# Optimization experiments

Hardware: AMD Instinct MI355X
Metric: run time of the kernel (lower is better)

The kernel has to match this reference:

```python
import jax, jax.numpy as jnp
import numpy as np

B, S, D, H, F = 4, 1024, 1024, 16, 4096
DH = D // H  # 64


def _xavier(key, shape):
    fan_in, fan_out = shape[-2], shape[-1]
    limit = np.sqrt(6.0 / (fan_in + fan_out)).astype(np.float32)
    return jax.random.uniform(key, shape, jnp.float32, -limit, limit)


def setup_inputs() -> dict:
    key = jax.random.key(0)
    ks = jax.random.split(key, 24)
    inp = {
        'decoder_input': jax.random.normal(ks[0], (B, S, D), jnp.float32),
        'encoder_output': jax.random.normal(ks[1], (B, S, D), jnp.float32),
        'mask': jnp.broadcast_to(jnp.tril(jnp.ones((S, S), jnp.bool_)), (B, S, S)),
    }
    # self-attention per-head Q/K/V weights stacked over heads: (H, D, DH)
    for i, p in enumerate(['sa', 'ca']):
        base = 2 + i * 8
        inp[f'{p}_wq'] = _xavier(ks[base + 0], (H, D, DH))
        inp[f'{p}_wk'] = _xavier(ks[base + 1], (H, D, DH))
        inp[f'{p}_wv'] = _xavier(ks[base + 2], (H, D, DH))
        inp[f'{p}_bq'] = jnp.zeros((H, DH), jnp.float32)
        inp[f'{p}_bk'] = jnp.zeros((H, DH), jnp.float32)
        inp[f'{p}_bv'] = jnp.zeros((H, DH), jnp.float32)
        inp[f'{p}_wo'] = _xavier(ks[base + 3], (H * DH, D))
        inp[f'{p}_bo'] = jnp.zeros((D,), jnp.float32)
    inp['ff_w1'] = _xavier(ks[18], (D, F))
    inp['ff_b1'] = jnp.zeros((F,), jnp.float32)
    inp['ff_w2'] = _xavier(ks[19], (F, D))
    inp['ff_b2'] = jnp.zeros((D,), jnp.float32)
    for j in (1, 2, 3):
        inp[f'ln{j}_g'] = jnp.ones((D,), jnp.float32)
        inp[f'ln{j}_b'] = jnp.zeros((D,), jnp.float32)
    return inp


def _layernorm(x, g, b, eps=1e-12):
    # torch x.var() default is unbiased (ddof=1) -- match it
    mean = jnp.mean(x, axis=-1, keepdims=True)
    var = jnp.var(x, axis=-1, keepdims=True, ddof=1)
    return g * (x - mean) * jax.lax.rsqrt(var + eps) + b


def _mha(q_in, k_in, v_in, wq, bq, wk, bk, wv, bv, wo, bo, mask=None):
    scale = np.float32(1.0 / np.sqrt(DH))
    q = jnp.einsum('bsd,hde->bhse', q_in, wq) + bq[None, :, None, :]
    k = jnp.einsum('bsd,hde->bhse', k_in, wk) + bk[None, :, None, :]
    v = jnp.einsum('bsd,hde->bhse', v_in, wv) + bv[None, :, None, :]
    scores = jnp.einsum('bhqe,bhke->bhqk', q, k) * scale
    if mask is not None:
        scores = jnp.where(mask[:, None, :, :], scores, jnp.float32(-1e9))
    attn = jax.nn.softmax(scores, axis=-1)
    out = jnp.einsum('bhqk,bhke->bhqe', attn, v)  # (B,H,S,DH)
    out = out.transpose(0, 2, 1, 3).reshape(q_in.shape[0], q_in.shape[1], H * DH)
    return out @ wo + bo


def reference(decoder_input, encoder_output, mask,
              sa_wq, sa_wk, sa_wv, sa_bq, sa_bk, sa_bv, sa_wo, sa_bo,
              ca_wq, ca_wk, ca_wv, ca_bq, ca_bk, ca_bv, ca_wo, ca_bo,
              ff_w1, ff_b1, ff_w2, ff_b2,
              ln1_g, ln1_b, ln2_g, ln2_b, ln3_g, ln3_b):
    # dropout is identity (eval mode)
    out1 = _mha(decoder_input, decoder_input, decoder_input,
                sa_wq, sa_bq, sa_wk, sa_bk, sa_wv, sa_bv, sa_wo, sa_bo, mask)
    out1 = _layernorm(out1 + decoder_input, ln1_g, ln1_b)
    out2 = _mha(out1, encoder_output, encoder_output,
                ca_wq, ca_bq, ca_wk, ca_bk, ca_wv, ca_bv, ca_wo, ca_bo, None)
    out2 = _layernorm(out2 + out1, ln2_g, ln2_b)
    out3 = jax.nn.relu(out2 @ ff_w1 + ff_b1) @ ff_w2 + ff_b2
    out3 = _layernorm(out3 + out2, ln3_g, ln3_b)
    return out3
```

## Files before the change

kernel.cpp:

```cpp
#include <hip/hip_runtime.h>
#include <hip/hip_bf16.h>

using bf16 = __hip_bfloat16;
typedef __attribute__((ext_vector_type(8))) short bf16x8;
typedef __attribute__((ext_vector_type(4))) float f32x4;

__device__ __forceinline__ float toF(float x) { return x; }
__device__ __forceinline__ float toF(bf16 x) { return __bfloat162float(x); }

template <typename T> __device__ __forceinline__ T fromF(float x);
template <> __device__ __forceinline__ float fromF<float>(float x) { return x; }
template <> __device__ __forceinline__ bf16 fromF<bf16>(float x) { return __float2bfloat16(x); }

__device__ __forceinline__ unsigned short f2bu(float f) {
    bf16 h = __float2bfloat16(f);
    return *reinterpret_cast<unsigned short*>(&h);
}

__global__ __launch_bounds__(256) void cvt_k(const float* __restrict__ X,
                                             unsigned short* __restrict__ Y, int n)
{
    int i = (blockIdx.x * 256 + threadIdx.x) * 4;
    if (i >= n) return;
    float4 v = *(const float4*)(X + i);
    ushort4 o;
    o.x = f2bu(v.x); o.y = f2bu(v.y); o.z = f2bu(v.z); o.w = f2bu(v.w);
    *(ushort4*)(Y + i) = o;
}

template <bool HEADED>
__global__ __launch_bounds__(256) void wtrans_k(
    const float* __restrict__ W, unsigned short* __restrict__ Wt, int K, int N)
{
    __shared__ float t[32][33];
    const int k0 = blockIdx.x * 32, n0 = blockIdx.y * 32;
    const int tx = threadIdx.x & 31, ty = threadIdx.x >> 5;
#pragma unroll
    for (int i = 0; i < 4; i++) {
        int k = k0 + ty + 8 * i, n = n0 + tx;
        float v;
        if constexpr (HEADED) v = W[((size_t)(n >> 6) * K + k) * 64 + (n & 63)];
        else                  v = W[(size_t)k * N + n];
        t[ty + 8 * i][tx] = v;
    }
    __syncthreads();
#pragma unroll
    for (int i = 0; i < 4; i++)
        Wt[(size_t)(n0 + ty + 8 * i) * K + k0 + tx] = f2bu(t[tx][ty + 8 * i]);
}

template <typename TO, typename TR, bool RELU, bool HASRES, bool TRANSC, bool NARROW>
__global__ __launch_bounds__(256) void gemm_mfma(
    const unsigned short* __restrict__ A, const unsigned short* __restrict__ Bt,
    const float* __restrict__ bias, const TR* __restrict__ res,
    TO* __restrict__ C, int M, int N, int K)
{
    constexpr int P = 56;
    constexpr int BN = NARROW ? 64 : 128;
    constexpr int MI = NARROW ? 2 : 4;
    __shared__ __align__(16) unsigned short As[128 * P];
    __shared__ __align__(16) unsigned short Bs[BN * P];

    const int tid = threadIdx.x;
    const int lane = tid & 63, wv = tid >> 6;
    const int quad = lane >> 4, col = lane & 15;
    const int m0 = blockIdx.y * 128, n0 = blockIdx.x * BN;
    const int wm = NARROW ? wv * 32 : (wv >> 1) * 64;
    const int wn = NARROW ? 0 : (wv & 1) * 64;

    f32x4 acc[MI][4];
#pragma unroll
    for (int i = 0; i < MI; i++)
#pragma unroll
        for (int j = 0; j < 4; j++) acc[i][j] = (f32x4){0.f, 0.f, 0.f, 0.f};

    const int r0 = tid >> 2;
    const int sg = (tid & 3) * 8;

    for (int k0 = 0; k0 < K; k0 += 32) {
        bf16x8 a0 = *(const bf16x8*)(A  + (size_t)(m0 + r0)      * K + k0 + sg);
        bf16x8 a1 = *(const bf16x8*)(A  + (size_t)(m0 + 64 + r0) * K + k0 + sg);
        bf16x8 b0 = *(const bf16x8*)(Bt + (size_t)(n0 + r0)      * K + k0 + sg);
        bf16x8 b1{};
        if constexpr (!NARROW)
            b1 = *(const bf16x8*)(Bt + (size_t)(n0 + 64 + r0) * K + k0 + sg);
        __syncthreads();
        *(bf16x8*)(As + r0 * P + sg)        = a0;
        *(bf16x8*)(As + (64 + r0) * P + sg) = a1;
        *(bf16x8*)(Bs + r0 * P + sg)        = b0;
        if constexpr (!NARROW)
            *(bf16x8*)(Bs + (64 + r0) * P + sg) = b1;
        __syncthreads();

        bf16x8 af[MI], bf[4];
#pragma unroll
        for (int mi = 0; mi < MI; mi++)
            af[mi] = *(const bf16x8*)(As + (wm + mi * 16 + col) * P + quad * 8);
#pragma unroll
        for (int ni = 0; ni < 4; ni++)
            bf[ni] = *(const bf16x8*)(Bs + (wn + ni * 16 + col) * P + quad * 8);
#pragma unroll
        for (int mi = 0; mi < MI; mi++)
#pragma unroll
            for (int ni = 0; ni < 4; ni++)
                acc[mi][ni] = __builtin_amdgcn_mfma_f32_16x16x32_bf16(
                    af[mi], bf[ni], acc[mi][ni], 0, 0, 0);
    }

    float bv[4];
#pragma unroll
    for (int ni = 0; ni < 4; ni++) bv[ni] = bias[n0 + wn + ni * 16 + col];
#pragma unroll
    for (int mi = 0; mi < MI; mi++) {
#pragma unroll
        for (int r = 0; r < 4; r++) {
            int m = m0 + wm + mi * 16 + quad * 4 + r;
#pragma unroll
            for (int ni = 0; ni < 4; ni++) {
                int n = n0 + wn + ni * 16 + col;
                float v = acc[mi][ni][r] + bv[ni];
                if constexpr (HASRES) v += toF(res[(size_t)m * N + n]);
                if constexpr (RELU) v = v > 0.f ? v : 0.f;
                if constexpr (TRANSC)
                    C[((size_t)(m >> 10) * 1024 + n) * 1024 + (m & 1023)] = fromF<TO>(v);
                else
                    C[(size_t)m * N + n] = fromF<TO>(v);
            }
        }
    }
}

struct SegArgs {
    const float* bias[3];
    unsigned short* out[3];
};

__global__ __launch_bounds__(256) void gemm_seg(
    const unsigned short* __restrict__ A, const unsigned short* __restrict__ Bt,
    SegArgs sp, int M, int K, int transSeg)
{
    constexpr int P = 56;
    __shared__ __align__(16) unsigned short As[128 * P];
    __shared__ __align__(16) unsigned short Bs[128 * P];

    const int tid = threadIdx.x;
    const int lane = tid & 63, wv = tid >> 6;
    const int quad = lane >> 4, col = lane & 15;
    const int m0 = blockIdx.y * 128, n0 = blockIdx.x * 128;
    const int wm = (wv >> 1) * 64, wn = (wv & 1) * 64;

    f32x4 acc[4][4];
#pragma unroll
    for (int i = 0; i < 4; i++)
#pragma unroll
        for (int j = 0; j < 4; j++) acc[i][j] = (f32x4){0.f, 0.f, 0.f, 0.f};

    const int r0 = tid >> 2;
    const int sg = (tid & 3) * 8;

    for (int k0 = 0; k0 < K; k0 += 32) {
        bf16x8 a0 = *(const bf16x8*)(A  + (size_t)(m0 + r0)      * K + k0 + sg);
        bf16x8 a1 = *(const bf16x8*)(A  + (size_t)(m0 + 64 + r0) * K + k0 + sg);
        bf16x8 b0 = *(const bf16x8*)(Bt + (size_t)(n0 + r0)      * K + k0 + sg);
        bf16x8 b1 = *(const bf16x8*)(Bt + (size_t)(n0 + 64 + r0) * K + k0 + sg);
        __syncthreads();
        *(bf16x8*)(As + r0 * P + sg)        = a0;
        *(bf16x8*)(As + (64 + r0) * P + sg) = a1;
        *(bf16x8*)(Bs + r0 * P + sg)        = b0;
        *(bf16x8*)(Bs + (64 + r0) * P + sg) = b1;
        __syncthreads();

        bf16x8 af[4], bf[4];
#pragma unroll
        for (int mi = 0; mi < 4; mi++)
            af[mi] = *(const bf16x8*)(As + (wm + mi * 16 + col) * P + quad * 8);
#pragma unroll
        for (int ni = 0; ni < 4; ni++)
            bf[ni] = *(const bf16x8*)(Bs + (wn + ni * 16 + col) * P + quad * 8);
#pragma unroll
        for (int mi = 0; mi < 4; mi++)
#pragma unroll
            for (int ni = 0; ni < 4; ni++)
                acc[mi][ni] = __builtin_amdgcn_mfma_f32_16x16x32_bf16(
                    af[mi], bf[ni], acc[mi][ni], 0, 0, 0);
    }

    const int seg = n0 >> 10;
    const float* bias = sp.bias[seg];
    unsigned short* out = sp.out[seg];
    const int nb = (n0 & 1023) + wn;
    const bool trans = (seg == transSeg);

    float bv[4];
#pragma unroll
    for (int ni = 0; ni < 4; ni++) bv[ni] = bias[nb + ni * 16 + col];
#pragma unroll
    for (int mi = 0; mi < 4; mi++) {
#pragma unroll
        for (int r = 0; r < 4; r++) {
            int m = m0 + wm + mi * 16 + quad * 4 + r;
#pragma unroll
            for (int ni = 0; ni < 4; ni++) {
                int nl = nb + ni * 16 + col;
                float v = acc[mi][ni][r] + bv[ni];
                if (trans)
                    out[((size_t)(m >> 10) * 1024 + nl) * 1024 + (m & 1023)] = f2bu(v);
                else
                    out[(size_t)m * 1024 + nl] = f2bu(v);
            }
        }
    }
}

template <bool CAUSAL>
__global__ __launch_bounds__(256) void fattn_k(
    const unsigned short* __restrict__ Q, const unsigned short* __restrict__ K,
    const unsigned short* __restrict__ Vt, unsigned short* __restrict__ O, int S)
{
    const int qt = blockIdx.x, h = blockIdx.y, b = blockIdx.z;
    const int H64 = 1024;
    const int tid = threadIdx.x;
    const int w = tid >> 6, lane = tid & 63;
    const int quad = lane >> 4, col = lane & 15;

    __shared__ __align__(16) unsigned short Ks[64 * 72];
    __shared__ __align__(16) unsigned short Vs[64 * 72];
    __shared__ __align__(16) unsigned short Ps[4 * 16 * 72];

    const int qBase = qt * 64 + w * 16;
    const size_t qrow = ((size_t)b * S + qBase + col) * H64 + h * 64;
    const bf16x8 qf0 = *(const bf16x8*)(Q + qrow + quad * 8);
    const bf16x8 qf1 = *(const bf16x8*)(Q + qrow + quad * 8 + 32);

    f32x4 o[4];
#pragma unroll
    for (int g = 0; g < 4; g++) o[g] = (f32x4){0.f, 0.f, 0.f, 0.f};
    float m_run[4], l_run[4];
#pragma unroll
    for (int r = 0; r < 4; r++) { m_run[r] = -1e30f; l_run[r] = 0.f; }

    const int skey = tid >> 2;
    const int sseg = (tid & 3) * 16;
    const size_t kgbase = (size_t)b * S * H64 + h * 64;
    const size_t vgbase = ((size_t)b * 1024 + h * 64) * (size_t)S;

    const int nkt = CAUSAL ? (qt + 1) : (S >> 6);
    const float scale = 0.125f;
    unsigned short* Pw = Ps + w * (16 * 72);

    for (int kt = 0; kt < nkt; kt++) {
        __syncthreads();
        {
            const unsigned short* kg_ = K + kgbase + (size_t)(kt * 64 + skey) * H64;
            const unsigned short* vg_ = Vt + vgbase + (size_t)skey * S + kt * 64;
            *(uint4*)(Ks + skey * 72 + sseg)     = *(const uint4*)(kg_ + sseg);
            *(uint4*)(Ks + skey * 72 + sseg + 8) = *(const uint4*)(kg_ + sseg + 8);
            *(uint4*)(Vs + skey * 72 + sseg)     = *(const uint4*)(vg_ + sseg);
            *(uint4*)(Vs + skey * 72 + sseg + 8) = *(const uint4*)(vg_ + sseg + 8);
        }
        __syncthreads();

        f32x4 s[4];
#pragma unroll
        for (int kg = 0; kg < 4; kg++) {
            bf16x8 k0 = *(const bf16x8*)(Ks + (kg * 16 + col) * 72 + quad * 8);
            bf16x8 k1 = *(const bf16x8*)(Ks + (kg * 16 + col) * 72 + quad * 8 + 32);
            f32x4 a = (f32x4){0.f, 0.f, 0.f, 0.f};
            a = __builtin_amdgcn_mfma_f32_16x16x32_bf16(qf0, k0, a, 0, 0, 0);
            a = __builtin_amdgcn_mfma_f32_16x16x32_bf16(qf1, k1, a, 0, 0, 0);
            s[kg] = a;
        }

#pragma unroll
        for (int kg = 0; kg < 4; kg++)
#pragma unroll
            for (int r = 0; r < 4; r++) {
                float v = s[kg][r] * scale;
                if (CAUSAL) {
                    int key = kt * 64 + kg * 16 + col;
                    int q = qBase + quad * 4 + r;
                    if (key > q) v = -1e30f;
                }
                s[kg][r] = v;
            }

#pragma unroll
        for (int r = 0; r < 4; r++) {
            float mx = fmaxf(fmaxf(s[0][r], s[1][r]), fmaxf(s[2][r], s[3][r]));
#pragma unroll
            for (int off = 1; off < 16; off <<= 1)
                mx = fmaxf(mx, __shfl_xor(mx, off));
            float mnew = fmaxf(m_run[r], mx);
            float ps = 0.f;
#pragma unroll
            for (int kg = 0; kg < 4; kg++) {
                float e = __expf(s[kg][r] - mnew);
                s[kg][r] = e;
                ps += e;
            }
#pragma unroll
            for (int off = 1; off < 16; off <<= 1)
                ps += __shfl_xor(ps, off);
            float alpha = __expf(m_run[r] - mnew);
            l_run[r] = l_run[r] * alpha + ps;
            m_run[r] = mnew;
#pragma unroll
            for (int g = 0; g < 4; g++) o[g][r] *= alpha;
        }

#pragma unroll
        for (int kg = 0; kg < 4; kg++)
#pragma unroll
            for (int r = 0; r < 4; r++)
                Pw[(quad * 4 + r) * 72 + kg * 16 + col] = f2bu(s[kg][r]);
        __syncthreads();

        bf16x8 p0 = *(const bf16x8*)(Pw + col * 72 + quad * 8);
        bf16x8 p1 = *(const bf16x8*)(Pw + col * 72 + quad * 8 + 32);

#pragma unroll
        for (int g = 0; g < 4; g++) {
            bf16x8 v0 = *(const bf16x8*)(Vs + (g * 16 + col) * 72 + quad * 8);
            bf16x8 v1 = *(const bf16x8*)(Vs + (g * 16 + col) * 72 + quad * 8 + 32);
            o[g] = __builtin_amdgcn_mfma_f32_16x16x32_bf16(p0, v0, o[g], 0, 0, 0);
            o[g] = __builtin_amdgcn_mfma_f32_16x16x32_bf16(p1, v1, o[g], 0, 0, 0);
        }
    }

    const size_t orow = ((size_t)b * S + qBase) * H64 + h * 64;
#pragma unroll
    for (int r = 0; r < 4; r++) {
        float inv = 1.f / l_run[r];
        int q = quad * 4 + r;
#pragma unroll
        for (int g = 0; g < 4; g++)
            O[orow + (size_t)q * H64 + g * 16 + col] = f2bu(o[g][r] * inv);
    }
}

template <typename TO>
__global__ __launch_bounds__(256) void ln_k(
    const float* __restrict__ X, const float* __restrict__ g,
    const float* __restrict__ bb, TO* __restrict__ O, int D)
{
    const int row = blockIdx.x;
    const int tid = threadIdx.x;
    __shared__ float xs[1024];
    __shared__ float red[256];
    const float* x = X + (size_t)row * D;

    float s = 0.f;
    for (int i = tid; i < D; i += 256) { float v = x[i]; xs[i] = v; s += v; }
    red[tid] = s;
    __syncthreads();
    for (int t = 128; t > 0; t >>= 1) {
        if (tid < t) red[tid] += red[tid + t];
        __syncthreads();
    }
    const float mean = red[0] / (float)D;
    __syncthreads();

    float s2 = 0.f;
    for (int i = tid; i < D; i += 256) { float d = xs[i] - mean; s2 += d * d; }
    red[tid] = s2;
    __syncthreads();
    for (int t = 128; t > 0; t >>= 1) {
        if (tid < t) red[tid] += red[tid + t];
        __syncthreads();
    }
    const float rstd = rsqrtf(red[0] / (float)(D - 1) + 1e-12f);

    TO* o = O + (size_t)row * D;
    for (int i = tid; i < D; i += 256)
        o[i] = fromF<TO>(g[i] * (xs[i] - mean) * rstd + bb[i]);
}

extern "C" void kernel_launch(void* const* d_in, const int* in_sizes, int n_in,
                              void* d_out, int out_size, void* d_ws, size_t ws_size,
                              hipStream_t stream)
{
    const int Bb = 4, S = 1024, D = 1024, F = 4096;
    const int M = Bb * S;
    const int H = 16;

    const float* dec = (const float*)d_in[0];
    const float* enc = (const float*)d_in[1];

    int base = 2;
    if (n_in >= 29 && in_sizes[2] == Bb * S * S) base = 3;

    const float* sa_wq = (const float*)d_in[base + 0];
    const float* sa_wk = (const float*)d_in[base + 1];
    const float* sa_wv = (const float*)d_in[base + 2];
    const float* sa_bq = (const float*)d_in[base + 3];
    const float* sa_bk = (const float*)d_in[base + 4];
    const float* sa_bv = (const float*)d_in[base + 5];
    const float* sa_wo = (const float*)d_in[base + 6];
    const float* sa_bo = (const float*)d_in[base + 7];
    const float* ca_wq = (const float*)d_in[base + 8];
    const float* ca_wk = (const float*)d_in[base + 9];
    const float* ca_wv = (const float*)d_in[base + 10];
    const float* ca_bq = (const float*)d_in[base + 11];
    const float* ca_bk = (const float*)d_in[base + 12];
    const float* ca_bv = (const float*)d_in[base + 13];
    const float* ca_wo = (const float*)d_in[base + 14];
    const float* ca_bo = (const float*)d_in[base + 15];
    const float* ff_w1 = (const float*)d_in[base + 16];
    const float* ff_b1 = (const float*)d_in[base + 17];
    const float* ff_w2 = (const float*)d_in[base + 18];
    const float* ff_b2 = (const float*)d_in[base + 19];
    const float* ln1_g = (const float*)d_in[base + 20];
    const float* ln1_b = (const float*)d_in[base + 21];
    const float* ln2_g = (const float*)d_in[base + 22];
    const float* ln2_b = (const float*)d_in[base + 23];
    const float* ln3_g = (const float*)d_in[base + 24];
    const float* ln3_b = (const float*)d_in[base + 25];

    const size_t E = (size_t)M * D;
    const size_t M1 = (size_t)1024 * 1024;
    float* SUM = (float*)d_ws;
    bf16* O1 = (bf16*)(SUM + E);
    bf16* O2 = O1 + E;
    bf16* Q  = O2 + E;
    bf16* Kb = Q + E;
    bf16* Vt = Kb + E;
    bf16* AO = Vt + E;
    bf16* HID = Q;
    unsigned short* decB = (unsigned short*)AO;
    unsigned short* Wt   = (unsigned short*)d_out;
    unsigned short* encB = (unsigned short*)d_out + 4 * 1024 * 1024;

    dim3 blk(256);
    dim3 gQKV(3 * D / 128, M / 128);
    dim3 gKV(2 * D / 128, M / 128);
    dim3 gN(D / 64, M / 128);
    dim3 gF(F / 128, M / 128);
    dim3 gA(S / 64, H, Bb);
    dim3 gT(D / 32, D / 32);
    dim3 gT1(D / 32, F / 32);
    dim3 gT2(F / 32, D / 32);

    cvt_k<<<M * D / 1024, blk, 0, stream>>>(dec, decB, M * D);
    cvt_k<<<M * D / 1024, blk, 0, stream>>>(enc, encB, M * D);

    wtrans_k<true><<<gT, blk, 0, stream>>>(sa_wq, Wt, D, D);
    wtrans_k<true><<<gT, blk, 0, stream>>>(sa_wk, Wt + M1, D, D);
    wtrans_k<true><<<gT, blk, 0, stream>>>(sa_wv, Wt + 2 * M1, D, D);
    {
        SegArgs sp;
        sp.bias[0] = sa_bq; sp.bias[1] = sa_bk; sp.bias[2] = sa_bv;
        sp.out[0] = (unsigned short*)Q; sp.out[1] = (unsigned short*)Kb;
        sp.out[2] = (unsigned short*)Vt;
        gemm_seg<<<gQKV, blk, 0, stream>>>(decB, Wt, sp, M, D, 2);
    }
    fattn_k<true><<<gA, blk, 0, stream>>>((const unsigned short*)Q, (const unsigned short*)Kb,
                                          (const unsigned short*)Vt, (unsigned short*)AO, S);
    wtrans_k<false><<<gT, blk, 0, stream>>>(sa_wo, Wt, D, D);
    gemm_mfma<float, float, false, true, false, true><<<gN, blk, 0, stream>>>(
        (const unsigned short*)AO, Wt, sa_bo, dec, SUM, M, D, D);
    ln_k<bf16><<<M, blk, 0, stream>>>(SUM, ln1_g, ln1_b, O1, D);

    wtrans_k<true><<<gT, blk, 0, stream>>>(ca_wq, Wt, D, D);
    gemm_mfma<bf16, float, false, false, false, true><<<gN, blk, 0, stream>>>(
        (const unsigned short*)O1, Wt, ca_bq, (const float*)nullptr, Q, M, D, D);
    wtrans_k<true><<<gT, blk, 0, stream>>>(ca_wk, Wt, D, D);
    wtrans_k<true><<<gT, blk, 0, stream>>>(ca_wv, Wt + M1, D, D);
    {
        SegArgs sp;
        sp.bias[0] = ca_bk; sp.bias[1] = ca_bv; sp.bias[2] = nullptr;
        sp.out[0] = (unsigned short*)Kb; sp.out[1] = (unsigned short*)Vt;
        sp.out[2] = nullptr;
        gemm_seg<<<gKV, blk, 0, stream>>>(encB, Wt, sp, M, D, 1);
    }
    fattn_k<false><<<gA, blk, 0, stream>>>((const unsigned short*)Q, (const unsigned short*)Kb,
                                           (const unsigned short*)Vt, (unsigned short*)AO, S);
    wtrans_k<false><<<gT, blk, 0, stream>>>(ca_wo, Wt, D, D);
    gemm_mfma<float, bf16, false, true, false, true><<<gN, blk, 0, stream>>>(
        (const unsigned short*)AO, Wt, ca_bo, O1, SUM, M, D, D);
    ln_k<bf16><<<M, blk, 0, stream>>>(SUM, ln2_g, ln2_b, O2, D);

    wtrans_k<false><<<gT1, blk, 0, stream>>>(ff_w1, Wt, D, F);
    gemm_mfma<bf16, float, true, false, false, false><<<gF, blk, 0, stream>>>(
        (const unsigned short*)O2, Wt, ff_b1, (const float*)nullptr, HID, M, F, D);
    wtrans_k<false><<<gT2, blk, 0, stream>>>(ff_w2, Wt, F, D);
    gemm_mfma<float, bf16, false, true, false, true><<<gN, blk, 0, stream>>>(
        (const unsigned short*)HID, Wt, ff_b2, O2, SUM, M, D, F);
    ln_k<float><<<M, blk, 0, stream>>>(SUM, ln3_g, ln3_b, (float*)d_out, D);
}
```

Before: 655.9 us.

## Use direct global-to-LDS loads with XOR swizzle and BK=64 in GEMMs

```diff
diff --git a/kernel.cpp b/kernel.cpp
--- a/kernel.cpp
+++ b/kernel.cpp
@@ -15,6 +15,12 @@
 __device__ __forceinline__ unsigned short f2bu(float f) {
     bf16 h = __float2bfloat16(f);
     return *reinterpret_cast<unsigned short*>(&h);
+}
+
+__device__ __forceinline__ void gload16(const unsigned short* g, unsigned short* l) {
+    __builtin_amdgcn_global_load_lds(
+        (const __attribute__((address_space(1))) unsigned int*)g,
+        (__attribute__((address_space(3))) unsigned int*)l, 16, 0, 0);
 }
 
 __global__ __launch_bounds__(256) void cvt_k(const float* __restrict__ X,
@@ -49,24 +55,22 @@
         Wt[(size_t)(n0 + ty + 8 * i) * K + k0 + tx] = f2bu(t[tx][ty + 8 * i]);
 }
 
-template <typename TO, typename TR, bool RELU, bool HASRES, bool TRANSC, bool NARROW>
+template <typename TO, typename TR, bool RELU, bool HASRES, int BN>
 __global__ __launch_bounds__(256) void gemm_mfma(
     const unsigned short* __restrict__ A, const unsigned short* __restrict__ Bt,
     const float* __restrict__ bias, const TR* __restrict__ res,
     TO* __restrict__ C, int M, int N, int K)
 {
-    constexpr int P = 56;
-    constexpr int BN = NARROW ? 64 : 128;
-    constexpr int MI = NARROW ? 2 : 4;
-    __shared__ __align__(16) unsigned short As[128 * P];
-    __shared__ __align__(16) unsigned short Bs[BN * P];
+    constexpr int MI = (BN == 128) ? 4 : 2;
+    __shared__ __align__(16) unsigned short As[128 * 64];
+    __shared__ __align__(16) unsigned short Bs[BN * 64];
 
     const int tid = threadIdx.x;
     const int lane = tid & 63, wv = tid >> 6;
     const int quad = lane >> 4, col = lane & 15;
     const int m0 = blockIdx.y * 128, n0 = blockIdx.x * BN;
-    const int wm = NARROW ? wv * 32 : (wv >> 1) * 64;
-    const int wn = NARROW ? 0 : (wv & 1) * 64;
+    const int wm = (BN == 128) ? (wv >> 1) * 64 : wv * 32;
+    const int wn = (BN == 128) ? (wv & 1) * 64 : 0;
 
     f32x4 acc[MI][4];
 #pragma unroll
@@ -74,37 +78,42 @@
 #pragma unroll
         for (int j = 0; j < 4; j++) acc[i][j] = (f32x4){0.f, 0.f, 0.f, 0.f};
 
-    const int r0 = tid >> 2;
-    const int sg = (tid & 3) * 8;
-
-    for (int k0 = 0; k0 < K; k0 += 32) {
-        bf16x8 a0 = *(const bf16x8*)(A  + (size_t)(m0 + r0)      * K + k0 + sg);
-        bf16x8 a1 = *(const bf16x8*)(A  + (size_t)(m0 + 64 + r0) * K + k0 + sg);
-        bf16x8 b0 = *(const bf16x8*)(Bt + (size_t)(n0 + r0)      * K + k0 + sg);
-        bf16x8 b1{};
-        if constexpr (!NARROW)
-            b1 = *(const bf16x8*)(Bt + (size_t)(n0 + 64 + r0) * K + k0 + sg);
-        __syncthreads();
-        *(bf16x8*)(As + r0 * P + sg)        = a0;
-        *(bf16x8*)(As + (64 + r0) * P + sg) = a1;
-        *(bf16x8*)(Bs + r0 * P + sg)        = b0;
-        if constexpr (!NARROW)
-            *(bf16x8*)(Bs + (64 + r0) * P + sg) = b1;
-        __syncthreads();
-
-        bf16x8 af[MI], bf[4];
-#pragma unroll
-        for (int mi = 0; mi < MI; mi++)
-            af[mi] = *(const bf16x8*)(As + (wm + mi * 16 + col) * P + quad * 8);
-#pragma unroll
-        for (int ni = 0; ni < 4; ni++)
-            bf[ni] = *(const bf16x8*)(Bs + (wn + ni * 16 + col) * P + quad * 8);
-#pragma unroll
-        for (int mi = 0; mi < MI; mi++)
+    const int rowl = (wv << 3) + (lane >> 3);
+    const int xq = (lane & 7) ^ (lane >> 3);
+    const unsigned short* Ag = A + (size_t)(m0 + rowl) * K + xq * 8;
+    const unsigned short* Bg = Bt + (size_t)(n0 + rowl) * K + xq * 8;
+    unsigned short* AsW = As + wv * 512;
+    unsigned short* BsW = Bs + wv * 512;
+
+    const int xr = col & 7;
+
+    for (int k0 = 0; k0 < K; k0 += 64) {
+        __syncthreads();
+#pragma unroll
+        for (int r = 0; r < 4; r++)
+            gload16(Ag + (size_t)(r * 32) * K + k0, AsW + r * 2048);
+#pragma unroll
+        for (int r = 0; r < BN / 32; r++)
+            gload16(Bg + (size_t)(r * 32) * K + k0, BsW + r * 2048);
+        __syncthreads();
+
+#pragma unroll
+        for (int kk = 0; kk < 2; kk++) {
+            const int cq = ((kk << 2) + quad) ^ xr;
+            bf16x8 af[MI], bfr[4];
+#pragma unroll
+            for (int mi = 0; mi < MI; mi++)
+                af[mi] = *(const bf16x8*)(As + (wm + mi * 16 + col) * 64 + cq * 8);
 #pragma unroll
             for (int ni = 0; ni < 4; ni++)
-                acc[mi][ni] = __builtin_amdgcn_mfma_f32_16x16x32_bf16(
-                    af[mi], bf[ni], acc[mi][ni], 0, 0, 0);
+                bfr[ni] = *(const bf16x8*)(Bs + (wn + ni * 16 + col) * 64 + cq * 8);
+#pragma unroll
+            for (int mi = 0; mi < MI; mi++)
+#pragma unroll
+                for (int ni = 0; ni < 4; ni++)
+                    acc[mi][ni] = __builtin_amdgcn_mfma_f32_16x16x32_bf16(
+                        af[mi], bfr[ni], acc[mi][ni], 0, 0, 0);
+        }
     }
 
     float bv[4];
@@ -121,10 +130,7 @@
                 float v = acc[mi][ni][r] + bv[ni];
                 if constexpr (HASRES) v += toF(res[(size_t)m * N + n]);
                 if constexpr (RELU) v = v > 0.f ? v : 0.f;
-                if constexpr (TRANSC)
-                    C[((size_t)(m >> 10) * 1024 + n) * 1024 + (m & 1023)] = fromF<TO>(v);
-                else
-                    C[(size_t)m * N + n] = fromF<TO>(v);
+                C[(size_t)m * N + n] = fromF<TO>(v);
             }
         }
     }
@@ -139,9 +145,8 @@
     const unsigned short* __restrict__ A, const unsigned short* __restrict__ Bt,
     SegArgs sp, int M, int K, int transSeg)
 {
-    constexpr int P = 56;
-    __shared__ __align__(16) unsigned short As[128 * P];
-    __shared__ __align__(16) unsigned short Bs[128 * P];
+    __shared__ __align__(16) unsigned short As[128 * 64];
+    __shared__ __align__(16) unsigned short Bs[128 * 64];
 
     const int tid = threadIdx.x;
     const int lane = tid & 63, wv = tid >> 6;
@@ -155,34 +160,41 @@
 #pragma unroll
         for (int j = 0; j < 4; j++) acc[i][j] = (f32x4){0.f, 0.f, 0.f, 0.f};
 
-    const int r0 = tid >> 2;
-    const int sg = (tid & 3) * 8;
-
-    for (int k0 = 0; k0 < K; k0 += 32) {
-        bf16x8 a0 = *(const bf16x8*)(A  + (size_t)(m0 + r0)      * K + k0 + sg);
-        bf16x8 a1 = *(const bf16x8*)(A  + (size_t)(m0 + 64 + r0) * K + k0 + sg);
-        bf16x8 b0 = *(const bf16x8*)(Bt + (size_t)(n0 + r0)      * K + k0 + sg);
-        bf16x8 b1 = *(const bf16x8*)(Bt + (size_t)(n0 + 64 + r0) * K + k0 + sg);
-        __syncthreads();
-        *(bf16x8*)(As + r0 * P + sg)        = a0;
-        *(bf16x8*)(As + (64 + r0) * P + sg) = a1;
-        *(bf16x8*)(Bs + r0 * P + sg)        = b0;
-        *(bf16x8*)(Bs + (64 + r0) * P + sg) = b1;
-        __syncthreads();
-
-        bf16x8 af[4], bf[4];
-#pragma unroll
-        for (int mi = 0; mi < 4; mi++)
-            af[mi] = *(const bf16x8*)(As + (wm + mi * 16 + col) * P + quad * 8);
-#pragma unroll
-        for (int ni = 0; ni < 4; ni++)
-            bf[ni] = *(const bf16x8*)(Bs + (wn + ni * 16 + col) * P + quad * 8);
-#pragma unroll
-        for (int mi = 0; mi < 4; mi++)
+    const int rowl = (wv << 3) + (lane >> 3);
+    const int xq = (lane & 7) ^ (lane >> 3);
+    const unsigned short* Ag = A + (size_t)(m0 + rowl) * K + xq * 8;
+    const unsigned short* Bg = Bt + (size_t)(n0 + rowl) * K + xq * 8;
+    unsigned short* AsW = As + wv * 512;
+    unsigned short* BsW = Bs + wv * 512;
+    const int xr = col & 7;
+
+    for (int k0 = 0; k0 < K; k0 += 64) {
+        __syncthreads();
+#pragma unroll
+        for (int r = 0; r < 4; r++)
+            gload16(Ag + (size_t)(r * 32) * K + k0, AsW + r * 2048);
+#pragma unroll
+        for (int r = 0; r < 4; r++)
+            gload16(Bg + (size_t)(r * 32) * K + k0, BsW + r * 2048);
+        __syncthreads();
+
+#pragma unroll
+        for (int kk = 0; kk < 2; kk++) {
+            const int cq = ((kk << 2) + quad) ^ xr;
+            bf16x8 af[4], bfr[4];
+#pragma unroll
+            for (int mi = 0; mi < 4; mi++)
+                af[mi] = *(const bf16x8*)(As + (wm + mi * 16 + col) * 64 + cq * 8);
 #pragma unroll
             for (int ni = 0; ni < 4; ni++)
-                acc[mi][ni] = __builtin_amdgcn_mfma_f32_16x16x32_bf16(
-                    af[mi], bf[ni], acc[mi][ni], 0, 0, 0);
+                bfr[ni] = *(const bf16x8*)(Bs + (wn + ni * 16 + col) * 64 + cq * 8);
+#pragma unroll
+            for (int mi = 0; mi < 4; mi++)
+#pragma unroll
+                for (int ni = 0; ni < 4; ni++)
+                    acc[mi][ni] = __builtin_amdgcn_mfma_f32_16x16x32_bf16(
+                        af[mi], bfr[ni], acc[mi][ni], 0, 0, 0);
+        }
     }
 
     const int seg = n0 >> 10;
@@ -456,12 +468,12 @@
     fattn_k<true><<<gA, blk, 0, stream>>>((const unsigned short*)Q, (const unsigned short*)Kb,
                                           (const unsigned short*)Vt, (unsigned short*)AO, S);
     wtrans_k<false><<<gT, blk, 0, stream>>>(sa_wo, Wt, D, D);
-    gemm_mfma<float, float, false, true, false, true><<<gN, blk, 0, stream>>>(
+    gemm_mfma<float, float, false, true, 64><<<gN, blk, 0, stream>>>(
         (const unsigned short*)AO, Wt, sa_bo, dec, SUM, M, D, D);
     ln_k<bf16><<<M, blk, 0, stream>>>(SUM, ln1_g, ln1_b, O1, D);
 
     wtrans_k<true><<<gT, blk, 0, stream>>>(ca_wq, Wt, D, D);
-    gemm_mfma<bf16, float, false, false, false, true><<<gN, blk, 0, stream>>>(
+    gemm_mfma<bf16, float, false, false, 64><<<gN, blk, 0, stream>>>(
         (const unsigned short*)O1, Wt, ca_bq, (const float*)nullptr, Q, M, D, D);
     wtrans_k<true><<<gT, blk, 0, stream>>>(ca_wk, Wt, D, D);
     wtrans_k<true><<<gT, blk, 0, stream>>>(ca_wv, Wt + M1, D, D);
@@ -475,15 +487,15 @@
     fattn_k<false><<<gA, blk, 0, stream>>>((const unsigned short*)Q, (const unsigned short*)Kb,
                                            (const unsigned short*)Vt, (unsigned short*)AO, S);
     wtrans_k<false><<<gT, blk, 0, stream>>>(ca_wo, Wt, D, D);
-    gemm_mfma<float, bf16, false, true, false, true><<<gN, blk, 0, stream>>>(
+    gemm_mfma<float, bf16, false, true, 64><<<gN, blk, 0, stream>>>(
         (const unsigned short*)AO, Wt, ca_bo, O1, SUM, M, D, D);
     ln_k<bf16><<<M, blk, 0, stream>>>(SUM, ln2_g, ln2_b, O2, D);
 
     wtrans_k<false><<<gT1, blk, 0, stream>>>(ff_w1, Wt, D, F);
-    gemm_mfma<bf16, float, true, false, false, false><<<gF, blk, 0, stream>>>(
+    gemm_mfma<bf16, float, true, false, 128><<<gF, blk, 0, stream>>>(
         (const unsigned short*)O2, Wt, ff_b1, (const float*)nullptr, HID, M, F, D);
     wtrans_k<false><<<gT2, blk, 0, stream>>>(ff_w2, Wt, F, D);
-    gemm_mfma<float, bf16, false, true, false, true><<<gN, blk, 0, stream>>>(
+    gemm_mfma<float, bf16, false, true, 64><<<gN, blk, 0, stream>>>(
         (const unsigned short*)HID, Wt, ff_b2, O2, SUM, M, D, F);
     ln_k<float><<<M, blk, 0, stream>>>(SUM, ln3_g, ln3_b, (float*)d_out, D);
 }
```

After: 610.9 us. 6.9% less time.
